# Kernel optimization log

Hardware: AMD Instinct MI355X
Metric: run time of the kernel (lower is better)

The kernel has to match this reference:

```python
import jax, jax.numpy as jnp
import numpy as np

B, T, I, H, D = 4, 4096, 1024, 16, 64


def setup_inputs() -> dict:
    key = jax.random.key(0)
    k1, k2, k3 = jax.random.split(key, 3)
    inputs = jax.random.normal(k1, (B, T, I), dtype=jnp.float32)
    kv_kernel = jax.random.normal(k2, (I, H, D, 2), dtype=jnp.float32) * (1.0 / np.sqrt(I))
    q_kernel = jax.random.normal(k3, (H, D), dtype=jnp.float32) * (1.0 / np.sqrt(D))
    return {"inputs": inputs, "kv_kernel": kv_kernel, "q_kernel": q_kernel}


def _combine(a, b):
    # state layout along last axis: [m (1), u (1), w (D)]
    ma, ua, wa = a[..., :1], a[..., 1:2], a[..., 2:]
    mb, ub, wb = b[..., :1], b[..., 1:2], b[..., 2:]
    m = jnp.maximum(ma, mb)
    ea = jnp.exp(ma - m)
    eb = jnp.exp(mb - m)
    return jnp.concatenate([m, ua * ea + ub * eb, wa * ea + wb * eb], axis=-1)


def reference(inputs, kv_kernel, q_kernel):
    # inputs: (B,T,I); kv_kernel: (I,H,D,2); q_kernel: (H,D)
    kv = jnp.einsum('bti,ihdk->bthdk', inputs, kv_kernel)
    kv = jax.nn.silu(kv)
    k = kv[..., 0]  # (B,T,H,D)
    v = kv[..., 1]  # (B,T,H,D)
    st = jnp.einsum('hd,bthd->bth', q_kernel, k)[..., None]  # (B,T,H,1)
    u_init = jnp.ones_like(st)
    elems = jnp.concatenate([st, u_init, v], axis=-1)  # (B,T,H,2+D)
    o = jax.lax.associative_scan(_combine, elems, axis=1)
    c = o[..., 1:2]  # denominator (B,T,H,1)
    a = o[..., 2:]   # numerator   (B,T,H,D)
    h = a / c        # (B,T,H,D)
    # concat_heads=False -> mean over heads
    return jnp.mean(h, axis=-2)  # (B,T,D)
```

## Files before the change

### kernel.cpp

```cpp
#include <hip/hip_runtime.h>
#include <hip/hip_bf16.h>
#include <math.h>

constexpr int B_ = 4, T_ = 4096, I_ = 1024, H_ = 16, D_ = 64;
constexpr int M_ = B_ * T_;
constexpr int N_ = H_ * D_ * 2;
constexpr int C_ = 64;
constexpr int L_ = T_ / C_;
constexpr int NT_ = 16;

typedef __bf16 bf16x8 __attribute__((ext_vector_type(8)));
typedef float  f32x4  __attribute__((ext_vector_type(4)));

__device__ __forceinline__ float silu_f(float x) {
    return x / (1.0f + __expf(-x));
}

__device__ __forceinline__ ushort f2bf_u(float x) {
    unsigned u = __float_as_uint(x);
    unsigned r = (u + 0x7fffu + ((u >> 16) & 1u)) >> 16;
    return (ushort)r;
}
__device__ __forceinline__ float bfu2f(ushort u) {
    return __uint_as_float(((unsigned)u) << 16);
}

__device__ __forceinline__ void gload_lds16(const void* g, void* l) {
    __builtin_amdgcn_global_load_lds(
        (const __attribute__((address_space(1))) unsigned int*)g,
        (__attribute__((address_space(3))) unsigned int*)l, 16, 0, 0);
}

__device__ __forceinline__ int perm6(int n) {
    int l15 = n & 15, j = (n >> 4) & 3;
    return ((l15 >> 1) << 3) + (j << 1) + (l15 & 1);
}

__global__ __launch_bounds__(256) void convert_fused_kernel(
    const float* __restrict__ A,  ushort* __restrict__ A2,
    const float* __restrict__ Bm, ushort* __restrict__ B2T)
{
    __shared__ float tile[64][65];
    const int tid = threadIdx.x;
    if (blockIdx.x < 16384) {
        int idx = blockIdx.x * 256 + tid;
        int m  = idx >> 8;
        int kq = (idx & 255) * 4;
        float4 a = *reinterpret_cast<const float4*>(&A[(size_t)m * 1024 + kq]);
        ushort4 hi;
        hi.x = f2bf_u(a.x);
        hi.y = f2bf_u(a.y);
        hi.z = f2bf_u(a.z);
        hi.w = f2bf_u(a.w);
        *reinterpret_cast<ushort4*>(&A2[(size_t)m * 1024 + kq]) = hi;
    } else {
        int bk = blockIdx.x - 16384;
        const int k0 = (bk & 15) * 64;
        const int n0 = (bk >> 4) * 64;
        #pragma unroll
        for (int p = 0; p < 4; ++p) {
            int f = tid + p * 256;
            int r  = f >> 4;
            int c4 = (f & 15) * 4;
            float4 v = *reinterpret_cast<const float4*>(
                &Bm[(size_t)(k0 + r) * 2048 + n0 + c4]);
            tile[r][c4 + 0] = v.x; tile[r][c4 + 1] = v.y;
            tile[r][c4 + 2] = v.z; tile[r][c4 + 3] = v.w;
        }
        __syncthreads();
        #pragma unroll
        for (int p = 0; p < 4; ++p) {
            int f = tid + p * 256;
            int n  = f >> 4;
            int kq = (f & 15) * 4;
            int pn = perm6(n);
            ushort4 hi;
            hi.x = f2bf_u(tile[kq + 0][pn]);
            hi.y = f2bf_u(tile[kq + 1][pn]);
            hi.z = f2bf_u(tile[kq + 2][pn]);
            hi.w = f2bf_u(tile[kq + 3][pn]);
            *reinterpret_cast<ushort4*>(&B2T[(size_t)(n0 + n) * 1024 + k0 + kq]) = hi;
        }
    }
}

__device__ __forceinline__ int akof(int t) { return t * 64; }
__device__ __forceinline__ int bkof(int t) { return t * 64; }

#define BARRIER do { asm volatile("" ::: "memory"); \
    __builtin_amdgcn_s_barrier(); \
    asm volatile("" ::: "memory"); } while (0)
#define WAITLGKM asm volatile("s_waitcnt lgkmcnt(0)" ::: "memory")
#define WAITVM(n) asm volatile("s_waitcnt vmcnt(" #n ")" ::: "memory")

#define STAGE(gptr, kb, ldsoff, rs2) do { \
    gload_lds16((gptr) + (kb),         lds + (ldsoff) + tid * 8); \
    gload_lds16((gptr) + (kb) + (rs2), lds + (ldsoff) + 4096 + tid * 8); \
} while (0)

#define RDA(ab, i, kk) (*reinterpret_cast<const bf16x8*>((ab) + (i) * 1024 + ((kk) ? ck1 : ck0)))
#define RDB(bb, j, kk) (*reinterpret_cast<const bf16x8*>((bb) + (j) * 1024 + ((kk) ? ck1 : ck0)))

#define PH_READ_A(ab, ibase) do { \
    _Pragma("unroll") for (int i_ = 0; i_ < 4; ++i_) { \
        a[i_][0] = RDA(ab, (ibase) + i_, 0); \
        a[i_][1] = RDA(ab, (ibase) + i_, 1); } } while (0)
#define PH_READ_B(bb, breg, jbase) do { \
    _Pragma("unroll") for (int j_ = 0; j_ < 2; ++j_) { \
        breg[j_][0] = RDB(bb, (jbase) + j_, 0); \
        breg[j_][1] = RDB(bb, (jbase) + j_, 1); } } while (0)

#define QUAD(IH, BREG, JB) do { \
    __builtin_amdgcn_s_setprio(1); \
    _Pragma("unroll") for (int i_ = 0; i_ < 4; ++i_) \
    _Pragma("unroll") for (int j_ = 0; j_ < 2; ++j_) \
    _Pragma("unroll") for (int k_ = 0; k_ < 2; ++k_) \
        acc[(IH) + i_][(JB) + j_] = __builtin_amdgcn_mfma_f32_16x16x32_bf16( \
            a[i_][k_], BREG[j_][k_], acc[(IH) + i_][(JB) + j_], 0, 0, 0); \
    __builtin_amdgcn_s_setprio(0); \
} while (0)

__global__ __launch_bounds__(512, 2) void gemm_mfma8_kernel(
    const ushort* __restrict__ A2,
    const ushort* __restrict__ B2T,
    const float* __restrict__ qk,
    ushort* __restrict__ v_buf,
    float* __restrict__ s_buf,
    float* __restrict__ agg_m,
    float* __restrict__ agg_u,
    float* __restrict__ agg_w)
{
    __shared__ ushort lds[65536];
    __shared__ float spart[8][128];
    __shared__ float s_lds[2][256];

    const int bid = blockIdx.x;
    const int swz = (bid & 7) * 64 + (bid >> 3);
    const int bx  = swz >> 6;
    const int by  = swz & 63;
    const int m0  = by * 256;
    const int n0  = bx * 256;

    const int tid  = threadIdx.x;
    const int lane = tid & 63;
    const int wid  = tid >> 6;
    const int wr = wid >> 2, wc = wid & 3;
    const int l15 = lane & 15, lg = lane >> 4;

    const int row0 = tid >> 3;
    const int ch0  = (tid & 7) ^ (row0 & 7);
    const ushort* pA  = A2  + (size_t)(m0 + row0) * 1024 + ch0 * 8;
    const ushort* pB  = B2T + (size_t)(n0 + row0) * 1024 + ch0 * 8;
    const ushort* pA1 = pA + 128 * 1024;
    const ushort* pB1 = pB + 128 * 1024;

    const int ck0 = ((0 + lg) ^ (l15 & 7)) * 8;
    const int ck1 = ((4 + lg) ^ (l15 & 7)) * 8;
    const ushort* aB0 = lds + (wr * 128 + l15) * 64;
    const ushort* bB0 = lds + 16384 + (wc * 64 + l15) * 64;
    const ushort* aB1 = aB0 + 32768;
    const ushort* bB1 = bB0 + 32768;

    f32x4 acc[8][4];
    #pragma unroll
    for (int i = 0; i < 8; ++i)
        #pragma unroll
        for (int j = 0; j < 4; ++j)
            acc[i][j] = (f32x4){0.f, 0.f, 0.f, 0.f};
    bf16x8 a[4][2], b01[2][2], b23[2][2];

    {
        STAGE(pA,  akof(0), 0,             65536);
        STAGE(pA1, akof(0), 8192,          65536);
        STAGE(pB,  bkof(0), 16384,         65536);
        STAGE(pB1, bkof(0), 16384 + 8192,  65536);
        STAGE(pB,  bkof(1), 49152,         65536);
        STAGE(pA,  akof(1), 32768,         65536);
        WAITVM(4);
        BARRIER;
    }

    #pragma unroll 1
    for (int I = 0; I < NT_ / 2 - 1; ++I) {
        const int t1g = 2 * I + 1, t2g = 2 * I + 2, t3g = 2 * I + 3;
        const int ak1 = akof(t1g), bk1 = bkof(t1g);
        const int ak2 = akof(t2g), bk2 = bkof(t2g);
        const int ak3 = akof(t3g), bk3 = bkof(t3g);
        PH_READ_A(aB0, 0); PH_READ_B(bB0, b01, 0);
        STAGE(pA1, ak1, 32768 + 8192, 65536);
        BARRIER; WAITLGKM; QUAD(0, b01, 0); BARRIER;
        PH_READ_B(bB0, b23, 2);
        STAGE(pB1, bk1, 49152 + 8192, 65536);
        BARRIER; WAITLGKM; QUAD(0, b23, 2); BARRIER;
        PH_READ_A(aB0, 4);
        STAGE(pB, bk2, 16384, 65536);
        BARRIER; WAITLGKM; QUAD(4, b01, 0); BARRIER;
        STAGE(pA, ak2, 0, 65536);
        WAITVM(4);
        BARRIER; QUAD(4, b23, 2); BARRIER;
        PH_READ_A(aB1, 0); PH_READ_B(bB1, b01, 0);
        STAGE(pA1, ak2, 8192, 65536);
        BARRIER; WAITLGKM; QUAD(0, b01, 0); BARRIER;
        PH_READ_B(bB1, b23, 2);
        STAGE(pB1, bk2, 16384 + 8192, 65536);
        BARRIER; WAITLGKM; QUAD(0, b23, 2); BARRIER;
        PH_READ_A(aB1, 4);
        STAGE(pB, bk3, 49152, 65536);
        BARRIER; WAITLGKM; QUAD(4, b01, 0); BARRIER;
        STAGE(pA, ak3, 32768, 65536);
        WAITVM(4);
        BARRIER; QUAD(4, b23, 2); BARRIER;
    }

    {
        const int t1g = NT_ - 1;
        const int ak1 = akof(t1g), bk1 = bkof(t1g);
        PH_READ_A(aB0, 0); PH_READ_B(bB0, b01, 0);
        STAGE(pA1, ak1, 32768 + 8192, 65536);
        BARRIER; WAITLGKM; QUAD(0, b01, 0); BARRIER;
        PH_READ_B(bB0, b23, 2);
        STAGE(pB1, bk1, 49152 + 8192, 65536);
        BARRIER; WAITLGKM; QUAD(0, b23, 2); BARRIER;
        PH_READ_A(aB0, 4);
        BARRIER; WAITLGKM; QUAD(4, b01, 0); BARRIER;
        WAITVM(0);
        BARRIER; QUAD(4, b23, 2); BARRIER;
        PH_READ_A(aB1, 0); PH_READ_B(bB1, b01, 0);
        BARRIER; WAITLGKM; QUAD(0, b01, 0); BARRIER;
        PH_READ_B(bB1, b23, 2);
        BARRIER; WAITLGKM; QUAD(0, b23, 2); BARRIER;
        PH_READ_A(aB1, 4);
        BARRIER; WAITLGKM; QUAD(4, b01, 0); BARRIER;
        QUAD(4, b23, 2);
    }

    const int hloc  = wc >> 1;
    const int h     = 2 * bx + hloc;
    const int dbase = (wc & 1) * 32 + (l15 >> 1) * 4;
    float qv[4];
    #pragma unroll
    for (int j = 0; j < 4; ++j) qv[j] = qk[h * 64 + dbase + j];
    const bool kcol = ((l15 & 1) == 0);

    #pragma unroll
    for (int i = 0; i < 8; ++i) {
        #pragma unroll
        for (int rr = 0; rr < 4; ++rr) {
            int rloc = wr * 128 + i * 16 + lg * 4 + rr;
            int m = m0 + rloc;
            int b = m >> 12, tt = m & 4095;
            float sv0 = silu_f(acc[i][0][rr]);
            float sv1 = silu_f(acc[i][1][rr]);
            float sv2 = silu_f(acc[i][2][rr]);
            float sv3 = silu_f(acc[i][3][rr]);
            float p = 0.f;
            if (kcol) {
                p = qv[0] * sv0 + qv[1] * sv1 + qv[2] * sv2 + qv[3] * sv3;
            } else {
                ushort4 vs4;
                vs4.x = f2bf_u(sv0); vs4.y = f2bf_u(sv1);
                vs4.z = f2bf_u(sv2); vs4.w = f2bf_u(sv3);
                *reinterpret_cast<ushort4*>(
                    &v_buf[((size_t)(b * H_ + h) * T_ + tt) * D_ + dbase]) = vs4;
            }
            p += __shfl_xor(p, 2);
            p += __shfl_xor(p, 4);
            p += __shfl_xor(p, 8);
            if (l15 == 0) spart[wid][i * 16 + lg * 4 + rr] = p;
        }
    }
    __syncthreads();
    {
        int wr2 = tid >> 8, hl = (tid >> 7) & 1, row = tid & 127;
        int m = m0 + wr2 * 128 + row;
        int b = m >> 12, tt = m & 4095;
        float sval = spart[wr2 * 4 + hl * 2][row] + spart[wr2 * 4 + hl * 2 + 1][row];
        s_buf[(size_t)(b * H_ + 2 * bx + hl) * T_ + tt] = sval;
        s_lds[hl][wr2 * 128 + row] = sval;
    }
    __syncthreads();

    {
        const int b  = m0 >> 12;
        #pragma unroll
        for (int cc = 0; cc < 2; ++cc) {
            const int c_l = wr * 2 + cc;
            const int cg  = ((m0 & 4095) >> 6) + c_l;
            float mm = -INFINITY, u = 0.f;
            float w0 = 0.f, w1 = 0.f, w2 = 0.f, w3 = 0.f;
            #pragma unroll
            for (int ir = 0; ir < 4; ++ir) {
                #pragma unroll
                for (int rr = 0; rr < 4; ++rr) {
                    float s  = s_lds[hloc][c_l * 64 + ir * 16 + lg * 4 + rr];
                    float mn = fmaxf(mm, s);
                    float ea = __expf(mm - mn);
                    float eb = __expf(s - mn);
                    u  = u * ea + eb;
                    w0 = w0 * ea + silu_f(acc[cc * 4 + ir][0][rr]) * eb;
                    w1 = w1 * ea + silu_f(acc[cc * 4 + ir][1][rr]) * eb;
                    w2 = w2 * ea + silu_f(acc[cc * 4 + ir][2][rr]) * eb;
                    w3 = w3 * ea + silu_f(acc[cc * 4 + ir][3][rr]) * eb;
                    mm = mn;
                }
            }
            #pragma unroll
            for (int mk = 16; mk <= 32; mk <<= 1) {
                float om = __shfl_xor(mm, mk);
                float ou = __shfl_xor(u,  mk);
                float o0 = __shfl_xor(w0, mk);
                float o1 = __shfl_xor(w1, mk);
                float o2 = __shfl_xor(w2, mk);
                float o3 = __shfl_xor(w3, mk);
                float mn = fmaxf(mm, om);
                float ea = __expf(mm - mn);
                float eb = __expf(om - mn);
                u  = u * ea + ou * eb;
                w0 = w0 * ea + o0 * eb;
                w1 = w1 * ea + o1 * eb;
                w2 = w2 * ea + o2 * eb;
                w3 = w3 * ea + o3 * eb;
                mm = mn;
            }
            const int base = (b * H_ + h) * C_ + cg;
            if ((wc & 1) == 0 && lane == 0) {
                agg_m[base] = mm;
                agg_u[base] = u;
            }
            if (!kcol && lg == 0) {
                float4 wv = {w0, w1, w2, w3};
                *reinterpret_cast<float4*>(
                    &agg_w[(size_t)base * D_ + dbase]) = wv;
            }
        }
    }
}

#define TILE_M 128
#define TILE_N 128
#define TILE_K 16
__global__ __launch_bounds__(256) void gemm_kv_kernel(
    const float* __restrict__ A, const float* __restrict__ Bm,
    const float* __restrict__ q, ushort* __restrict__ v_buf,
    float* __restrict__ s_buf)
{
    __shared__ float As[TILE_K][TILE_M + 4];
    __shared__ float Bs[TILE_K][TILE_N + 4];
    const int tid = threadIdx.x;
    const int h   = blockIdx.x;
    const int bm  = blockIdx.y;
    const int m0  = bm * TILE_M;
    const int n0  = h * TILE_N;
    const int tx = tid & 15, ty = tid >> 4;
    float acc[8][8];
    #pragma unroll
    for (int i = 0; i < 8; ++i)
        #pragma unroll
        for (int j = 0; j < 8; ++j) acc[i][j] = 0.f;
    for (int k0 = 0; k0 < I_; k0 += TILE_K) {
        #pragma unroll
        for (int p = 0; p < 2; ++p) {
            int f = tid + p * 256;
            int row = f >> 2, kq = (f & 3) * 4;
            float4 av = *reinterpret_cast<const float4*>(
                &A[(size_t)(m0 + row) * I_ + k0 + kq]);
            As[kq + 0][row] = av.x; As[kq + 1][row] = av.y;
            As[kq + 2][row] = av.z; As[kq + 3][row] = av.w;
        }
        #pragma unroll
        for (int p = 0; p < 2; ++p) {
            int f = tid + p * 256;
            int row = f >> 5, c4 = (f & 31) * 4;
            *reinterpret_cast<float4*>(&Bs[row][c4]) =
                *reinterpret_cast<const float4*>(
                    &Bm[(size_t)(k0 + row) * N_ + n0 + c4]);
        }
        __syncthreads();
        #pragma unroll
        for (int kk = 0; kk < TILE_K; ++kk) {
            float4 a0 = *reinterpret_cast<const float4*>(&As[kk][ty * 8]);
            float4 a1 = *reinterpret_cast<const float4*>(&As[kk][ty * 8 + 4]);
            float4 b0 = *reinterpret_cast<const float4*>(&Bs[kk][tx * 8]);
            float4 b1 = *reinterpret_cast<const float4*>(&Bs[kk][tx * 8 + 4]);
            float af[8] = {a0.x, a0.y, a0.z, a0.w, a1.x, a1.y, a1.z, a1.w};
            float bf[8] = {b0.x, b0.y, b0.z, b0.w, b1.x, b1.y, b1.z, b1.w};
            #pragma unroll
            for (int i = 0; i < 8; ++i)
                #pragma unroll
                for (int j = 0; j < 8; ++j)
                    acc[i][j] = fmaf(af[i], bf[j], acc[i][j]);
        }
        __syncthreads();
    }
    float4 qv = *reinterpret_cast<const float4*>(&q[h * D_ + tx * 4]);
    float qf[4] = {qv.x, qv.y, qv.z, qv.w};
    #pragma unroll
    for (int i = 0; i < 8; ++i) {
        int m = m0 + ty * 8 + i;
        int b = m >> 12, t = m & 4095;
        float partial = 0.f;
        #pragma unroll
        for (int j = 0; j < 4; ++j) {
            float kval = silu_f(acc[i][2 * j]);
            float vv = silu_f(acc[i][2 * j + 1]);
            v_buf[((size_t)(b * H_ + h) * T_ + t) * D_ + tx * 4 + j] = f2bf_u(vv);
            partial = fmaf(qf[j], kval, partial);
        }
        #pragma unroll
        for (int mask = 8; mask >= 1; mask >>= 1)
            partial += __shfl_xor(partial, mask, 16);
        if (tx == 0) s_buf[(size_t)(b * H_ + h) * T_ + t] = partial;
    }
}

__global__ __launch_bounds__(64) void chunk_agg_kernel(
    const float* __restrict__ s_buf, const ushort* __restrict__ v_buf,
    float* __restrict__ agg_m, float* __restrict__ agg_u,
    float* __restrict__ agg_w)
{
    const int x    = blockIdx.x;
    const int c    = x & (C_ - 1);
    const int bh   = x >> 6;
    const int lane = threadIdx.x;
    const float* sp  = s_buf + (size_t)bh * T_ + c * L_;
    const ushort* vp = v_buf + ((size_t)bh * T_ + c * L_) * D_ + lane;
    float m = -INFINITY, u = 0.f, w = 0.f;
    for (int t = 0; t < L_; ++t) {
        float s  = sp[t];
        float vv = bfu2f(vp[(size_t)t * D_]);
        float mn = fmaxf(m, s);
        float ea = __expf(m - mn);
        float eb = __expf(s - mn);
        u = u * ea + eb;
        w = w * ea + vv * eb;
        m = mn;
    }
    if (lane == 0) { agg_m[x] = m; agg_u[x] = u; }
    agg_w[(size_t)x * D_ + lane] = w;
}

__global__ __launch_bounds__(64) void chunk_prefix_kernel(
    float* __restrict__ agg_m, float* __restrict__ agg_u,
    float* __restrict__ agg_w)
{
    const int bh   = blockIdx.x;
    const int lane = threadIdx.x;
    float pm = -INFINITY, pu = 0.f, pw = 0.f;
    #pragma unroll 4
    for (int c = 0; c < C_; ++c) {
        int base = bh * C_ + c;
        float am = agg_m[base];
        float au = agg_u[base];
        float aw = agg_w[(size_t)base * D_ + lane];
        if (lane == 0) { agg_m[base] = pm; agg_u[base] = pu; }
        agg_w[(size_t)base * D_ + lane] = pw;
        float mn = fmaxf(pm, am);
        float ea = __expf(pm - mn);
        float eb = __expf(am - mn);
        pu = pu * ea + au * eb;
        pw = pw * ea + aw * eb;
        pm = mn;
    }
}

__global__ __launch_bounds__(256) void scan_apply_kernel(
    const float* __restrict__ s_buf, const ushort* __restrict__ v_buf,
    const float* __restrict__ agg_m, const float* __restrict__ agg_u,
    const float* __restrict__ agg_w, float* __restrict__ out)
{
    __shared__ float part[4][8][64];
    const int bx   = blockIdx.x;
    const int b    = bx >> 6;
    const int c    = bx & (C_ - 1);
    const int w    = threadIdx.x >> 6;
    const int lane = threadIdx.x & 63;
    float m[4], u[4], ws[4];
    #pragma unroll
    for (int j = 0; j < 4; ++j) {
        int h = w * 4 + j;
        int base = (b * H_ + h) * C_ + c;
        m[j]  = agg_m[base];
        u[j]  = agg_u[base];
        ws[j] = agg_w[(size_t)base * D_ + lane];
    }
    const int t0 = c * L_;
    for (int g = 0; g < L_ / 8; ++g) {
        #pragma unroll
        for (int qq = 0; qq < 8; ++qq) {
            int t = t0 + g * 8 + qq;
            float acc = 0.f;
            #pragma unroll
            for (int j = 0; j < 4; ++j) {
                int h = w * 4 + j;
                size_t bht = (size_t)(b * H_ + h) * T_ + t;
                float s  = s_buf[bht];
                float vv = bfu2f(v_buf[bht * D_ + lane]);
                float mn = fmaxf(m[j], s);
                float ea = __expf(m[j] - mn);
                float eb = __expf(s - mn);
                u[j]  = u[j] * ea + eb;
                ws[j] = ws[j] * ea + vv * eb;
                m[j]  = mn;
                acc += ws[j] / u[j];
            }
            part[w][qq][lane] = acc;
        }
        __syncthreads();
        {
            int e  = threadIdx.x;
            int tt = e >> 6, d = e & 63;
            float sum = part[0][tt][d] + part[1][tt][d]
                      + part[2][tt][d] + part[3][tt][d];
            out[((size_t)b * T_ + (t0 + g * 8 + tt)) * D_ + d] = sum * (1.f / 16.f);
        }
        {
            int e  = threadIdx.x + 256;
            int tt = e >> 6, d = e & 63;
            float sum = part[0][tt][d] + part[1][tt][d]
                      + part[2][tt][d] + part[3][tt][d];
            out[((size_t)b * T_ + (t0 + g * 8 + tt)) * D_ + d] = sum * (1.f / 16.f);
        }
        __syncthreads();
    }
}

extern "C" void kernel_launch(void* const* d_in, const int* in_sizes, int n_in,
                              void* d_out, int out_size, void* d_ws, size_t ws_size,
                              hipStream_t stream) {
    const float* A  = (const float*)d_in[0];
    const float* Bm = (const float*)d_in[1];
    const float* q  = (const float*)d_in[2];
    float* out = (float*)d_out;

    ushort* v_buf = (ushort*)d_ws;
    float*  s_buf = (float*)(v_buf + (size_t)B_ * H_ * T_ * D_);
    float*  agg_m = s_buf + (size_t)B_ * H_ * T_;
    float*  agg_u = agg_m + B_ * H_ * C_;
    float*  agg_w = agg_u + B_ * H_ * C_;
    ushort* A2    = (ushort*)(agg_w + (size_t)B_ * H_ * C_ * D_);
    ushort* B2T   = A2 + (size_t)M_ * 1024;

    size_t need = (size_t)B_ * H_ * T_ * D_ * 2
                + ((size_t)262144 + 4096 + 4096 + 262144) * 4
                + ((size_t)M_ * 1024 + (size_t)2048 * 1024) * 2;

    if (ws_size >= need) {
        convert_fused_kernel<<<16896, 256, 0, stream>>>(A, A2, Bm, B2T);
        gemm_mfma8_kernel<<<512, 512, 0, stream>>>(A2, B2T, q, v_buf, s_buf,
                                                   agg_m, agg_u, agg_w);
    } else {
        dim3 ggrid(H_, M_ / TILE_M);
        gemm_kv_kernel<<<ggrid, 256, 0, stream>>>(A, Bm, q, v_buf, s_buf);
        chunk_agg_kernel<<<B_ * H_ * C_, 64, 0, stream>>>(s_buf, v_buf,
                                                          agg_m, agg_u, agg_w);
    }
    chunk_prefix_kernel<<<B_ * H_, 64, 0, stream>>>(agg_m, agg_u, agg_w);
    scan_apply_kernel<<<B_ * C_, 256, 0, stream>>>(s_buf, v_buf, agg_m, agg_u, agg_w, out);
}
```

Baseline: 148.0 us.

## Remap GEMM tiles per XCD and vectorize scan-apply lanes across heads

The GEMM block-to-tile mapping changes so each XCD gets a contiguous group of 8 M-tiles across all N-tiles, which should improve L2 reuse of the A rows. The scan-apply kernel now gives each wave 4 heads at once, with 16 lanes per head and each lane holding 4 D elements. Loads become vectorized ushort4/float4, the per-lane head loop is removed, and the division becomes a single reciprocal. Heads are reduced with cross-lane shuffles, and the final stores use float4. This cuts the serial per-lane recurrence work by 4x, at the cost of extra shuffles.

New measurement: 153.9 us. 1.04x slower.

```diff
diff --git a/kernel.cpp b/kernel.cpp
--- a/kernel.cpp
+++ b/kernel.cpp
@@ -135,9 +135,10 @@
     __shared__ float s_lds[2][256];
 
     const int bid = blockIdx.x;
-    const int swz = (bid & 7) * 64 + (bid >> 3);
-    const int bx  = swz >> 6;
-    const int by  = swz & 63;
+    const int xcd = bid & 7;
+    const int q   = bid >> 3;
+    const int by  = xcd * 8 + (q & 7);
+    const int bx  = q >> 3;
     const int m0  = by * 256;
     const int n0  = bx * 256;
 
@@ -474,51 +475,59 @@
     const int c    = bx & (C_ - 1);
     const int w    = threadIdx.x >> 6;
     const int lane = threadIdx.x & 63;
-    float m[4], u[4], ws[4];
-    #pragma unroll
-    for (int j = 0; j < 4; ++j) {
-        int h = w * 4 + j;
-        int base = (b * H_ + h) * C_ + c;
-        m[j]  = agg_m[base];
-        u[j]  = agg_u[base];
-        ws[j] = agg_w[(size_t)base * D_ + lane];
-    }
+    const int hsub = lane >> 4;
+    const int dg   = lane & 15;
+    const int h    = w * 4 + hsub;
+    const int base = (b * H_ + h) * C_ + c;
+
+    float m = agg_m[base];
+    float u = agg_u[base];
+    float4 w4 = *reinterpret_cast<const float4*>(&agg_w[(size_t)base * D_ + dg * 4]);
+
     const int t0 = c * L_;
+    const float*  sp = s_buf + (size_t)(b * H_ + h) * T_;
+    const ushort* vp = v_buf + ((size_t)(b * H_ + h) * T_) * D_ + dg * 4;
+
     for (int g = 0; g < L_ / 8; ++g) {
         #pragma unroll
         for (int qq = 0; qq < 8; ++qq) {
             int t = t0 + g * 8 + qq;
-            float acc = 0.f;
-            #pragma unroll
-            for (int j = 0; j < 4; ++j) {
-                int h = w * 4 + j;
-                size_t bht = (size_t)(b * H_ + h) * T_ + t;
-                float s  = s_buf[bht];
-                float vv = bfu2f(v_buf[bht * D_ + lane]);
-                float mn = fmaxf(m[j], s);
-                float ea = __expf(m[j] - mn);
-                float eb = __expf(s - mn);
-                u[j]  = u[j] * ea + eb;
-                ws[j] = ws[j] * ea + vv * eb;
-                m[j]  = mn;
-                acc += ws[j] / u[j];
+            float s = sp[t];
+            ushort4 vv = *reinterpret_cast<const ushort4*>(&vp[(size_t)t * D_]);
+            float mn = fmaxf(m, s);
+            float ea = __expf(m - mn);
+            float eb = __expf(s - mn);
+            u    = u    * ea + eb;
+            w4.x = w4.x * ea + bfu2f(vv.x) * eb;
+            w4.y = w4.y * ea + bfu2f(vv.y) * eb;
+            w4.z = w4.z * ea + bfu2f(vv.z) * eb;
+            w4.w = w4.w * ea + bfu2f(vv.w) * eb;
+            m = mn;
+            float ru = 1.0f / u;
+            float a0 = w4.x * ru, a1 = w4.y * ru, a2 = w4.z * ru, a3 = w4.w * ru;
+            a0 += __shfl_xor(a0, 16); a1 += __shfl_xor(a1, 16);
+            a2 += __shfl_xor(a2, 16); a3 += __shfl_xor(a3, 16);
+            a0 += __shfl_xor(a0, 32); a1 += __shfl_xor(a1, 32);
+            a2 += __shfl_xor(a2, 32); a3 += __shfl_xor(a3, 32);
+            if (hsub == 0) {
+                float4 av = {a0, a1, a2, a3};
+                *reinterpret_cast<float4*>(&part[w][qq][dg * 4]) = av;
             }
-            part[w][qq][lane] = acc;
         }
         __syncthreads();
-        {
-            int e  = threadIdx.x;
-            int tt = e >> 6, d = e & 63;
-            float sum = part[0][tt][d] + part[1][tt][d]
-                      + part[2][tt][d] + part[3][tt][d];
-            out[((size_t)b * T_ + (t0 + g * 8 + tt)) * D_ + d] = sum * (1.f / 16.f);
-        }
-        {
-            int e  = threadIdx.x + 256;
-            int tt = e >> 6, d = e & 63;
-            float sum = part[0][tt][d] + part[1][tt][d]
-                      + part[2][tt][d] + part[3][tt][d];
-            out[((size_t)b * T_ + (t0 + g * 8 + tt)) * D_ + d] = sum * (1.f / 16.f);
+        if (threadIdx.x < 128) {
+            int tt = threadIdx.x >> 4, dgg = threadIdx.x & 15;
+            float4 p0 = *reinterpret_cast<const float4*>(&part[0][tt][dgg * 4]);
+            float4 p1 = *reinterpret_cast<const float4*>(&part[1][tt][dgg * 4]);
+            float4 p2 = *reinterpret_cast<const float4*>(&part[2][tt][dgg * 4]);
+            float4 p3 = *reinterpret_cast<const float4*>(&part[3][tt][dgg * 4]);
+            float4 o;
+            o.x = (p0.x + p1.x + p2.x + p3.x) * (1.f / 16.f);
+            o.y = (p0.y + p1.y + p2.y + p3.y) * (1.f / 16.f);
+            o.z = (p0.z + p1.z + p2.z + p3.z) * (1.f / 16.f);
+            o.w = (p0.w + p1.w + p2.w + p3.w) * (1.f / 16.f);
+            *reinterpret_cast<float4*>(
+                &out[((size_t)b * T_ + (t0 + g * 8 + tt)) * D_ + dgg * 4]) = o;
         }
         __syncthreads();
     }
```
